# Optimization experiments

Hardware: AMD Instinct MI355X
Metric: run time of the kernel (lower is better)

The kernel has to match this reference:

```python
import jax, jax.numpy as jnp
import numpy as np

B, L, E, H = 2, 2048, 1024, 16
D = E // H  # 64


def setup_inputs() -> dict:
    key = jax.random.key(0)
    ks = jax.random.split(key, 9)
    return {
        "query": jax.random.normal(ks[0], (B, L, E), dtype=jnp.float32),
        "value": jax.random.normal(ks[1], (B, L, E), dtype=jnp.float32),
        "key": jax.random.normal(ks[2], (B, L, E), dtype=jnp.float32),
        "mask": jax.random.randint(ks[3], (B, 1, L, L), 0, 2, dtype=jnp.int32),
        "Wq": jax.random.normal(ks[4], (D, D), dtype=jnp.float32) * 0.05,
        "Wk": jax.random.normal(ks[5], (D, D), dtype=jnp.float32) * 0.05,
        "Wv": jax.random.normal(ks[6], (D, D), dtype=jnp.float32) * 0.05,
        "Wfc": jax.random.normal(ks[7], (E, E), dtype=jnp.float32) * 0.02,
        "bfc": jax.random.normal(ks[8], (E,), dtype=jnp.float32) * 0.02,
    }


def reference(query, value, key, mask, Wq, Wk, Wv, Wfc, bfc):
    b, q_len, _ = query.shape
    k_len = key.shape[1]
    v_len = value.shape[1]
    # split heads: [b, l, H, D]
    q = query.reshape(b, q_len, H, D)
    k = key.reshape(b, k_len, H, D)
    v = value.reshape(b, v_len, H, D)
    # per-head linear projections (shared weights across heads, no bias)
    q = jnp.einsum('bqhd,ed->bqhe', q, Wq)
    k = jnp.einsum('bkhd,ed->bkhe', k, Wk)
    v = jnp.einsum('bvhd,ed->bvhe', v, Wv)
    # attention scores [b, H, q, k]
    attn = jnp.einsum('bqhd,bkhd->bhqk', q, k)
    # NOTE: original masks BEFORE scaling, and scales by sqrt(embedding_size)
    attn = jnp.where(mask == 0, jnp.float32(-1e20), attn)
    attn = attn / jnp.float32(E ** 0.5)
    attn = jax.nn.softmax(attn, axis=3)
    out = jnp.einsum('bhqk,bkhd->bqhd', attn, v).reshape(b, q_len, E)
    out = out @ Wfc.T + bfc
    return out
```

## Files before the change

kernel.cpp:

```cpp
#include <hip/hip_runtime.h>
#include <hip/hip_bf16.h>


#define B_ 2
#define L_ 2048
#define E_ 1024
#define H_ 16
#define D_ 64

typedef __attribute__((ext_vector_type(8))) short s8v;
typedef __attribute__((ext_vector_type(4))) float f4v;
typedef __attribute__((ext_vector_type(2))) float f2v;

__device__ __forceinline__ f4v mfma16(s8v a, s8v b, f4v c) {
    return __builtin_amdgcn_mfma_f32_16x16x32_bf16(a, b, c, 0, 0, 0);
}

__device__ __forceinline__ float fast_exp2(float x) {
    return __builtin_amdgcn_exp2f(x);
}

__device__ __forceinline__ ushort bf16bits(float f) {
    __hip_bfloat16 h = __float2bfloat16(f);
    return *(ushort*)&h;
}

__device__ __forceinline__ void glds16(const __hip_bfloat16* g, ushort* l) {
    __builtin_amdgcn_global_load_lds(
        (const __attribute__((address_space(1))) void*)g,
        (__attribute__((address_space(3))) void*)l,
        16, 0, 0);
}

__device__ __forceinline__ s8v ld8_dual(const void* p, size_t idx, bool isf32) {
    if (isf32) {
        const float* pf = (const float*)p + idx;
        f4v f0 = *(const f4v*)pf;
        f4v f1 = *(const f4v*)(pf + 4);
        s8v r;
        r[0] = (short)bf16bits(f0[0]); r[1] = (short)bf16bits(f0[1]);
        r[2] = (short)bf16bits(f0[2]); r[3] = (short)bf16bits(f0[3]);
        r[4] = (short)bf16bits(f1[0]); r[5] = (short)bf16bits(f1[1]);
        r[6] = (short)bf16bits(f1[2]); r[7] = (short)bf16bits(f1[3]);
        return r;
    }
    return *(const s8v*)((const __hip_bfloat16*)p + idx);
}

__device__ __forceinline__ s8v ld8_ws(const __hip_bfloat16* p) {
    return *(const s8v*)p;
}

__device__ __forceinline__ s8v u4_to_s8(uint a, uint b, uint c, uint d) {
    union { uint u[4]; s8v v; } x;
    x.u[0] = a; x.u[1] = b; x.u[2] = c; x.u[3] = d;
    return x.v;
}

__device__ __forceinline__ bool block_detect_f32(const void* q_in, int* sflag) {
    if (threadIdx.x == 0) *sflag = 0;
    __syncthreads();
    const ushort* qq = (const ushort*)q_in + threadIdx.x * 16;
    int bad = 0;
    #pragma unroll
    for (int i = 0; i < 16; ++i) bad += (((qq[i] >> 7) & 0xFF) >= 0x8E);
    bad += __shfl_xor(bad, 1);
    bad += __shfl_xor(bad, 2);
    bad += __shfl_xor(bad, 4);
    bad += __shfl_xor(bad, 8);
    bad += __shfl_xor(bad, 16);
    bad += __shfl_xor(bad, 32);
    if ((threadIdx.x & 63) == 0) atomicAdd(sflag, bad);
    __syncthreads();
    return *sflag > 100;
}

__device__ __forceinline__ void cvt_piece(
    size_t i4, const void* Wfc, const void* bfc,
    __hip_bfloat16* wfc_bf, __hip_bfloat16* bfc_bf, bool isf32)
{
    const size_t base = i4 * 4;
    const size_t n1 = (size_t)E_ * E_;
    if (base >= n1 + E_) return;
    const void* src = (base < n1) ? Wfc : bfc;
    const size_t off = (base < n1) ? base : base - n1;
    __hip_bfloat16* dst = (base < n1) ? (wfc_bf + off) : (bfc_bf + off);
    if (isf32) {
        f4v v = *(const f4v*)((const float*)src + off);
        #pragma unroll
        for (int j = 0; j < 4; ++j) dst[j] = __float2bfloat16(v[j]);
    } else {
        *(ushort4*)dst = *(const ushort4*)((const ushort*)src + off);
    }
}

__global__ __launch_bounds__(256) void proj_all_kernel(
    const void* __restrict__ q_in, const void* __restrict__ k_in,
    const void* __restrict__ v_in,
    const void* __restrict__ Wq, const void* __restrict__ Wk,
    const void* __restrict__ Wv,
    const void* __restrict__ Wfc, const void* __restrict__ bfc,
    const int* __restrict__ mask, unsigned long long* __restrict__ mbits,
    __hip_bfloat16* __restrict__ qp, __hip_bfloat16* __restrict__ kp,
    __hip_bfloat16* __restrict__ vpT,
    __hip_bfloat16* __restrict__ wfc_bf, __hip_bfloat16* __restrict__ bfc_bf)
{
    __shared__ __align__(16) ushort tile[64][72];
    __shared__ __align__(16) ushort wlds[64 * 72];
    __shared__ int sflag;
    const int wave = threadIdx.x >> 6;
    const int lane = threadIdx.x & 63;
    const int quad = lane >> 4;
    const int l16  = lane & 15;

    if (blockIdx.y == 3) {
        const int lane_ = threadIdx.x & 63;
        const size_t wbase = (size_t)blockIdx.x * 128 + wave * 32;
        #pragma unroll 4
        for (int i = 0; i < 32; ++i) {
            const size_t widx = wbase + i;
            const int v = mask[widx * 64 + lane_];
            const unsigned long long bal = __ballot(v != 0);
            if (lane_ == 0) mbits[widx] = bal;
        }
        return;
    }

    const bool isf32 = block_detect_f32(q_in, &sflag);

    if (blockIdx.y == 4) {
        cvt_piece((size_t)blockIdx.x * 256 + threadIdx.x, Wfc, bfc, wfc_bf, bfc_bf, isf32);
        if (blockIdx.x == 0)
            cvt_piece((size_t)(E_ * (size_t)E_ / 4) + threadIdx.x, Wfc, bfc, wfc_bf, bfc_bf, isf32);
        return;
    }

    {
        const void* W = blockIdx.y == 0 ? Wq : (blockIdx.y == 1 ? Wk : Wv);
        const int row = threadIdx.x >> 2;
        const int c0  = (threadIdx.x & 3) * 16;
        if (isf32) {
            const float* wsrc = (const float*)W + row * 64 + c0;
            #pragma unroll
            for (int j = 0; j < 16; ++j)
                wlds[row * 72 + c0 + j] = bf16bits(wsrc[j]);
        } else {
            const ushort* wsrc = (const ushort*)W + row * 64 + c0;
            *(s8v*)&wlds[row * 72 + c0]     = *(const s8v*)wsrc;
            *(s8v*)&wlds[row * 72 + c0 + 8] = *(const s8v*)(wsrc + 8);
        }
    }
    __syncthreads();

    if (blockIdx.y < 2) {
        const void* X = blockIdx.y == 0 ? q_in : k_in;
        __hip_bfloat16* dst = blockIdx.y == 0 ? qp : kp;
        const float oscale = (blockIdx.y == 0) ? 0.045084439755930314f : 1.0f;
        const int m0 = (blockIdx.x * 4 + wave) * 16;

        const size_t abase = (size_t)(m0 + l16) * D_;
        s8v a0 = ld8_dual(X, abase + quad * 8, isf32);
        s8v a1 = ld8_dual(X, abase + 32 + quad * 8, isf32);

        f4v acc[4];
        #pragma unroll
        for (int nt = 0; nt < 4; ++nt) {
            const ushort* wr = &wlds[(nt * 16 + l16) * 72];
            s8v b0 = *(const s8v*)(wr + quad * 8);
            s8v b1 = *(const s8v*)(wr + 32 + quad * 8);
            f4v c = {0.f, 0.f, 0.f, 0.f};
            c = mfma16(a0, b0, c);
            c = mfma16(a1, b1, c);
            acc[nt] = c;
        }
        #pragma unroll
        for (int r = 0; r < 4; ++r) {
            const int m = m0 + quad * 4 + r;
            const int h = m & 15;
            const int bl = m >> 4;
            const int b = bl >> 11;
            const int l = bl & (L_ - 1);
            #pragma unroll
            for (int nt = 0; nt < 4; ++nt) {
                const int e = nt * 16 + l16;
                dst[(((size_t)(b * H_ + h)) * L_ + l) * D_ + e] =
                    __float2bfloat16(acc[nt][r] * oscale);
            }
        }
    } else {
        const int l0 = (blockIdx.x & 31) * 64;
        const int bh = blockIdx.x >> 5;
        const int b = bh >> 4, h = bh & 15;
        const int lw = l0 + wave * 16;

        const size_t xbase = ((size_t)(b * L_ + lw + l16)) * E_ + h * D_;
        s8v a0 = ld8_dual(v_in, xbase + quad * 8, isf32);
        s8v a1 = ld8_dual(v_in, xbase + 32 + quad * 8, isf32);

        #pragma unroll
        for (int nt = 0; nt < 4; ++nt) {
            const int e = nt * 16 + l16;
            const ushort* wr = &wlds[e * 72];
            s8v b0 = *(const s8v*)(wr + quad * 8);
            s8v b1 = *(const s8v*)(wr + 32 + quad * 8);
            f4v c = {0.f, 0.f, 0.f, 0.f};
            c = mfma16(a0, b0, c);
            c = mfma16(a1, b1, c);
            #pragma unroll
            for (int r = 0; r < 4; ++r)
                tile[wave * 16 + quad * 4 + r][e] = bf16bits(c[r]);
        }
        __syncthreads();
        const int e  = threadIdx.x >> 2;
        const int lc = (threadIdx.x & 3) * 16;
        s8v s0, s1;
        #pragma unroll
        for (int i = 0; i < 8; ++i) {
            s0[i] = (short)tile[lc + i][e];
            s1[i] = (short)tile[lc + 8 + i][e];
        }
        __hip_bfloat16* drow = vpT + ((size_t)bh * D_ + e) * L_ + l0 + lc;
        *(s8v*)drow = s0;
        *(s8v*)(drow + 8) = s1;
    }
}

__global__ __launch_bounds__(256) void cvt_wfc_kernel(
    const void* __restrict__ Wfc, const void* __restrict__ bfc,
    __hip_bfloat16* __restrict__ wfc_bf, __hip_bfloat16* __restrict__ bfc_bf,
    const void* __restrict__ q_in)
{
    __shared__ int sflag;
    const bool isf32 = block_detect_f32(q_in, &sflag);
    cvt_piece((size_t)blockIdx.x * 256 + threadIdx.x, Wfc, bfc, wfc_bf, bfc_bf, isf32);
}

__global__ __launch_bounds__(256, 4) void attn_kernel(
    const __hip_bfloat16* __restrict__ qp,
    const __hip_bfloat16* __restrict__ kp,
    const __hip_bfloat16* __restrict__ vpT,
    const unsigned long long* __restrict__ mbits,
    __hip_bfloat16* __restrict__ attn_out)
{
    __shared__ __align__(16) ushort kbuf[2][64 * 64];
    __shared__ __align__(16) ushort vbuf[2][64 * 64];

    const int wave = threadIdx.x >> 6;
    const int lane = threadIdx.x & 63;
    const int quad = lane >> 4;
    const int l16  = lane & 15;
    const int sw   = l16 & 7;
    const int bh = blockIdx.y;
    const int b = bh >> 4, h = bh & 15;
    const int q0 = blockIdx.x * 64 + wave * 16;

    const __hip_bfloat16* kbh = kp + (size_t)bh * L_ * D_;
    const __hip_bfloat16* vbh = vpT + (size_t)bh * D_ * L_;
    const unsigned long long* mrow = mbits + ((size_t)b * L_ + q0 + l16) * 32;

    const int lrow = lane >> 3;
    const int lchk = (lane & 7) ^ lrow;
    const int r0 = wave * 16;
    const __hip_bfloat16* kg0 = kbh + (size_t)(r0 + lrow) * D_ + lchk * 8;
    const __hip_bfloat16* kg1 = kbh + (size_t)(r0 + 8 + lrow) * D_ + lchk * 8;
    const __hip_bfloat16* vg0 = vbh + (size_t)(r0 + lrow) * L_ + lchk * 8;
    const __hip_bfloat16* vg1 = vbh + (size_t)(r0 + 8 + lrow) * L_ + lchk * 8;

    const __hip_bfloat16* qbase = qp + ((size_t)bh * L_ + q0) * D_;
    s8v qa0 = ld8_ws(qbase + (size_t)l16 * D_ + quad * 8);
    s8v qa1 = ld8_ws(qbase + (size_t)l16 * D_ + 32 + quad * 8);

    f2v rs2 = {0.f, 0.f};
    f4v o[4];
    #pragma unroll
    for (int nt = 0; nt < 4; ++nt) o[nt] = (f4v){0.f, 0.f, 0.f, 0.f};

    glds16(kg0, &kbuf[0][r0 * 64]);
    glds16(kg1, &kbuf[0][r0 * 64 + 512]);
    glds16(vg0, &vbuf[0][r0 * 64]);
    glds16(vg1, &vbuf[0][r0 * 64 + 512]);
    __syncthreads();

    const int shq = quad * 4;
    int cur = 0;
    for (int it = 0; it < 32; ++it) {
        const int k0 = it * 64;
        const unsigned long long wq = mrow[it];
        const uint wlo_sh = ((uint)wq) >> shq;
        const uint whi_sh = ((uint)(wq >> 32)) >> shq;
        if (it < 31) {
            glds16(kg0 + (size_t)(k0 + 64) * D_, &kbuf[cur ^ 1][r0 * 64]);
            glds16(kg1 + (size_t)(k0 + 64) * D_, &kbuf[cur ^ 1][r0 * 64 + 512]);
            glds16(vg0 + (k0 + 64), &vbuf[cur ^ 1][r0 * 64]);
            glds16(vg1 + (k0 + 64), &vbuf[cur ^ 1][r0 * 64 + 512]);
        }
        f4v s[4];
        #pragma unroll
        for (int nt = 0; nt < 4; ++nt) {
            const ushort* kr = &kbuf[cur][(nt * 16 + l16) * 64];
            s8v kb0 = *(const s8v*)(kr + ((quad ^ sw) << 3));
            s8v kb1 = *(const s8v*)(kr + (((quad + 4) ^ sw) << 3));
            f4v c = {0.f, 0.f, 0.f, 0.f};
            c = mfma16(kb0, qa0, c);
            c = mfma16(kb1, qa1, c);
            s[nt] = c;
        }
        uint dw[4][2];
        #pragma unroll
        for (int nt = 0; nt < 4; ++nt) {
            const uint hs = (nt & 2) ? whi_sh : wlo_sh;
            float pr[4];
            #pragma unroll
            for (int r = 0; r < 4; ++r) {
                const float p = fast_exp2(s[nt][r]);
                const int m = __builtin_amdgcn_sbfe((int)hs, ((nt & 1) << 4) + r, 1);
                pr[r] = __uint_as_float(__float_as_uint(p) & (uint)m);
            }
            rs2 += (f2v){pr[0], pr[1]};
            rs2 += (f2v){pr[2], pr[3]};
            asm("v_cvt_pk_bf16_f32 %0, %1, %2"
                : "=v"(dw[nt][0]) : "v"(pr[0]), "v"(pr[1]));
            asm("v_cvt_pk_bf16_f32 %0, %1, %2"
                : "=v"(dw[nt][1]) : "v"(pr[2]), "v"(pr[3]));
        }
        uint w00 = dw[0][0], w10 = dw[1][0];
        uint w01 = dw[0][1], w11 = dw[1][1];
        uint w20 = dw[2][0], w30 = dw[3][0];
        uint w21 = dw[2][1], w31 = dw[3][1];
        asm("v_permlane32_swap_b32 %0, %1" : "+v"(w00), "+v"(w10));
        asm("v_permlane16_swap_b32 %0, %1" : "+v"(w00), "+v"(w10));
        asm("v_permlane32_swap_b32 %0, %1" : "+v"(w01), "+v"(w11));
        asm("v_permlane16_swap_b32 %0, %1" : "+v"(w01), "+v"(w11));
        asm("v_permlane32_swap_b32 %0, %1" : "+v"(w20), "+v"(w30));
        asm("v_permlane16_swap_b32 %0, %1" : "+v"(w20), "+v"(w30));
        asm("v_permlane32_swap_b32 %0, %1" : "+v"(w21), "+v"(w31));
        asm("v_permlane16_swap_b32 %0, %1" : "+v"(w21), "+v"(w31));
        s8v pa0 = u4_to_s8(w00, w01, w10, w11);
        s8v pa1 = u4_to_s8(w20, w21, w30, w31);
        #pragma unroll
        for (int nt = 0; nt < 4; ++nt) {
            const ushort* vr = &vbuf[cur][(nt * 16 + l16) * 64];
            s8v vb0 = *(const s8v*)(vr + ((quad ^ sw) << 3));
            s8v vb1 = *(const s8v*)(vr + (((quad + 4) ^ sw) << 3));
            o[nt] = mfma16(pa0, vb0, o[nt]);
            o[nt] = mfma16(pa1, vb1, o[nt]);
        }
        __syncthreads();
        cur ^= 1;
    }
    float v = rs2[0] + rs2[1];
    v += __shfl_xor(v, 16, 64);
    v += __shfl_xor(v, 32, 64);
    #pragma unroll
    for (int r = 0; r < 4; ++r) {
        const int qrow = quad * 4 + r;
        const float li = __shfl(v, qrow, 64);
        const float inv = 1.0f / fmaxf(li, 1e-30f);
        const int row = q0 + qrow;
        #pragma unroll
        for (int nt = 0; nt < 4; ++nt) {
            const int d = nt * 16 + l16;
            attn_out[((size_t)(b * L_ + row)) * E_ + h * D_ + d] =
                __float2bfloat16(o[nt][r] * inv);
        }
    }
}

__global__ __launch_bounds__(256, 4) void fc_kernel(
    const __hip_bfloat16* __restrict__ x,
    const __hip_bfloat16* __restrict__ wfc_bf,
    const __hip_bfloat16* __restrict__ bfc_bf,
    void* __restrict__ out, const void* __restrict__ q_in)
{
    __shared__ __align__(16) ushort abuf[2][64 * 64];
    __shared__ __align__(16) ushort bbuf[2][64 * 64];
    __shared__ int sflag;
    const bool isf32 = block_detect_f32(q_in, &sflag);
    const int wave = threadIdx.x >> 6;
    const int lane = threadIdx.x & 63;
    const int quad = lane >> 4;
    const int l16  = lane & 15;
    const int sw   = l16 & 7;
    const int m0 = blockIdx.x * 64;
    const int n0 = blockIdx.y * 64;

    const int lrow = lane >> 3;
    const int lchk = (lane & 7) ^ lrow;
    const int r0 = wave * 16;
    const __hip_bfloat16* ag0 = x + (size_t)(m0 + r0 + lrow) * E_ + lchk * 8;
    const __hip_bfloat16* ag1 = x + (size_t)(m0 + r0 + 8 + lrow) * E_ + lchk * 8;
    const __hip_bfloat16* bg0 = wfc_bf + (size_t)(n0 + r0 + lrow) * E_ + lchk * 8;
    const __hip_bfloat16* bg1 = wfc_bf + (size_t)(n0 + r0 + 8 + lrow) * E_ + lchk * 8;

    f4v acc[4];
    #pragma unroll
    for (int nt = 0; nt < 4; ++nt) acc[nt] = (f4v){0.f, 0.f, 0.f, 0.f};

    glds16(ag0, &abuf[0][r0 * 64]);
    glds16(ag1, &abuf[0][r0 * 64 + 512]);
    glds16(bg0, &bbuf[0][r0 * 64]);
    glds16(bg1, &bbuf[0][r0 * 64 + 512]);
    __syncthreads();

    int cur = 0;
    for (int it = 0; it < 16; ++it) {
        const int k0 = it * 64;
        if (it < 15) {
            glds16(ag0 + k0 + 64, &abuf[cur ^ 1][r0 * 64]);
            glds16(ag1 + k0 + 64, &abuf[cur ^ 1][r0 * 64 + 512]);
            glds16(bg0 + k0 + 64, &bbuf[cur ^ 1][r0 * 64]);
            glds16(bg1 + k0 + 64, &bbuf[cur ^ 1][r0 * 64 + 512]);
        }
        const ushort* ar = &abuf[cur][(r0 + l16) * 64];
        s8v a0 = *(const s8v*)(ar + ((quad ^ sw) << 3));
        s8v a1 = *(const s8v*)(ar + (((quad + 4) ^ sw) << 3));
        #pragma unroll
        for (int nt = 0; nt < 4; ++nt) {
            const ushort* br = &bbuf[cur][(nt * 16 + l16) * 64];
            s8v b0 = *(const s8v*)(br + ((quad ^ sw) << 3));
            s8v b1 = *(const s8v*)(br + (((quad + 4) ^ sw) << 3));
            acc[nt] = mfma16(a0, b0, acc[nt]);
            acc[nt] = mfma16(a1, b1, acc[nt]);
        }
        __syncthreads();
        cur ^= 1;
    }
    #pragma unroll
    for (int r = 0; r < 4; ++r) {
        const int m = m0 + r0 + quad * 4 + r;
        #pragma unroll
        for (int nt = 0; nt < 4; ++nt) {
            const int n = n0 + nt * 16 + l16;
            const float val = acc[nt][r] + __bfloat162float(bfc_bf[n]);
            if (isf32) ((float*)out)[(size_t)m * E_ + n] = val;
            else       ((__hip_bfloat16*)out)[(size_t)m * E_ + n] = __float2bfloat16(val);
        }
    }
}

extern "C" void kernel_launch(void* const* d_in, const int* in_sizes, int n_in,
                              void* d_out, int out_size, void* d_ws, size_t ws_size,
                              hipStream_t stream) {
    const void* query = d_in[0];
    const void* value = d_in[1];
    const void* key   = d_in[2];
    const int*  mask  = (const int*)d_in[3];
    const void* Wq  = d_in[4];
    const void* Wk  = d_in[5];
    const void* Wv  = d_in[6];
    const void* Wfc = d_in[7];
    const void* bfc = d_in[8];

    char* ws = (char*)d_ws;
    unsigned long long* mbits     = (unsigned long long*)(ws + (64u << 10));
    __hip_bfloat16* qp            = (__hip_bfloat16*)(ws + (2u  << 20));
    __hip_bfloat16* kp            = (__hip_bfloat16*)(ws + (10u << 20));
    __hip_bfloat16* vpT           = (__hip_bfloat16*)(ws + (18u << 20));
    __hip_bfloat16* attn_out      = (__hip_bfloat16*)(ws + (26u << 20));

    const bool big_ws = ws_size >= (37ull << 20);
    __hip_bfloat16* wfc_bf = big_ws ? (__hip_bfloat16*)(ws + (34ull << 20)) : qp;
    __hip_bfloat16* bfc_bf = wfc_bf + (size_t)E_ * E_;

    proj_all_kernel<<<dim3(1024, big_ws ? 5 : 4), 256, 0, stream>>>(
        query, key, value, Wq, Wk, Wv, Wfc, bfc, mask, mbits,
        qp, kp, vpT, wfc_bf, bfc_bf);
    attn_kernel<<<dim3(32, 32), 256, 0, stream>>>(qp, kp, vpT, mbits, attn_out);
    if (!big_ws)
        cvt_wfc_kernel<<<1025, 256, 0, stream>>>(Wfc, bfc, wfc_bf, bfc_bf, query);
    fc_kernel<<<dim3(64, 16), 256, 0, stream>>>(attn_out, wfc_bf, bfc_bf, d_out, query);
}
```

Before: 222.0 us.

## Enlarge FC GEMM tiles to 128x128 and store Q/K projections row-major

The FC kernel moves from 64x64 tiles with 256 threads to 128x128 tiles with 512 threads. Each wave now computes a 64x32 sub-tile with 4x2 MFMA fragments, which raises operand reuse from LDS and cuts the block count. Separately, the Q/K projection outputs are written in the natural [b,l,h,d] layout, so the stores are contiguous. The attention kernel now reads them with stride E instead of per-head contiguous rows. The trade-offs are higher register pressure, more LDS per block, and fewer blocks (256) to fill the GPU.

```diff
diff --git a/kernel.cpp b/kernel.cpp
--- a/kernel.cpp
+++ b/kernel.cpp
@@ -60,7 +60,7 @@
 __device__ __forceinline__ bool block_detect_f32(const void* q_in, int* sflag) {
     if (threadIdx.x == 0) *sflag = 0;
     __syncthreads();
-    const ushort* qq = (const ushort*)q_in + threadIdx.x * 16;
+    const ushort* qq = (const ushort*)q_in + (threadIdx.x & 255) * 16;
     int bad = 0;
     #pragma unroll
     for (int i = 0; i < 16; ++i) bad += (((qq[i] >> 7) & 0xFF) >= 0x8E);
@@ -70,7 +70,7 @@
     bad += __shfl_xor(bad, 8);
     bad += __shfl_xor(bad, 16);
     bad += __shfl_xor(bad, 32);
-    if ((threadIdx.x & 63) == 0) atomicAdd(sflag, bad);
+    if ((threadIdx.x & 63) == 0 && threadIdx.x < 256) atomicAdd(sflag, bad);
     __syncthreads();
     return *sflag > 100;
 }
@@ -176,15 +176,10 @@
         #pragma unroll
         for (int r = 0; r < 4; ++r) {
             const int m = m0 + quad * 4 + r;
-            const int h = m & 15;
-            const int bl = m >> 4;
-            const int b = bl >> 11;
-            const int l = bl & (L_ - 1);
             #pragma unroll
             for (int nt = 0; nt < 4; ++nt) {
                 const int e = nt * 16 + l16;
-                dst[(((size_t)(b * H_ + h)) * L_ + l) * D_ + e] =
-                    __float2bfloat16(acc[nt][r] * oscale);
+                dst[(size_t)m * D_ + e] = __float2bfloat16(acc[nt][r] * oscale);
             }
         }
     } else {
@@ -254,21 +249,21 @@
     const int b = bh >> 4, h = bh & 15;
     const int q0 = blockIdx.x * 64 + wave * 16;
 
-    const __hip_bfloat16* kbh = kp + (size_t)bh * L_ * D_;
+    const __hip_bfloat16* kbh = kp + (size_t)b * L_ * E_ + h * D_;
     const __hip_bfloat16* vbh = vpT + (size_t)bh * D_ * L_;
     const unsigned long long* mrow = mbits + ((size_t)b * L_ + q0 + l16) * 32;
 
     const int lrow = lane >> 3;
     const int lchk = (lane & 7) ^ lrow;
     const int r0 = wave * 16;
-    const __hip_bfloat16* kg0 = kbh + (size_t)(r0 + lrow) * D_ + lchk * 8;
-    const __hip_bfloat16* kg1 = kbh + (size_t)(r0 + 8 + lrow) * D_ + lchk * 8;
+    const __hip_bfloat16* kg0 = kbh + (size_t)(r0 + lrow) * E_ + lchk * 8;
+    const __hip_bfloat16* kg1 = kbh + (size_t)(r0 + 8 + lrow) * E_ + lchk * 8;
     const __hip_bfloat16* vg0 = vbh + (size_t)(r0 + lrow) * L_ + lchk * 8;
     const __hip_bfloat16* vg1 = vbh + (size_t)(r0 + 8 + lrow) * L_ + lchk * 8;
 
-    const __hip_bfloat16* qbase = qp + ((size_t)bh * L_ + q0) * D_;
-    s8v qa0 = ld8_ws(qbase + (size_t)l16 * D_ + quad * 8);
-    s8v qa1 = ld8_ws(qbase + (size_t)l16 * D_ + 32 + quad * 8);
+    const __hip_bfloat16* qbase = qp + (size_t)b * L_ * E_ + h * D_ + (size_t)q0 * E_;
+    s8v qa0 = ld8_ws(qbase + (size_t)l16 * E_ + quad * 8);
+    s8v qa1 = ld8_ws(qbase + (size_t)l16 * E_ + 32 + quad * 8);
 
     f2v rs2 = {0.f, 0.f};
     f4v o[4];
@@ -289,8 +284,8 @@
         const uint wlo_sh = ((uint)wq) >> shq;
         const uint whi_sh = ((uint)(wq >> 32)) >> shq;
         if (it < 31) {
-            glds16(kg0 + (size_t)(k0 + 64) * D_, &kbuf[cur ^ 1][r0 * 64]);
-            glds16(kg1 + (size_t)(k0 + 64) * D_, &kbuf[cur ^ 1][r0 * 64 + 512]);
+            glds16(kg0 + (size_t)(k0 + 64) * E_, &kbuf[cur ^ 1][r0 * 64]);
+            glds16(kg1 + (size_t)(k0 + 64) * E_, &kbuf[cur ^ 1][r0 * 64 + 512]);
             glds16(vg0 + (k0 + 64), &vbuf[cur ^ 1][r0 * 64]);
             glds16(vg1 + (k0 + 64), &vbuf[cur ^ 1][r0 * 64 + 512]);
         }
@@ -366,14 +361,14 @@
     }
 }
 
-__global__ __launch_bounds__(256, 4) void fc_kernel(
+__global__ __launch_bounds__(512, 2) void fc_kernel(
     const __hip_bfloat16* __restrict__ x,
     const __hip_bfloat16* __restrict__ wfc_bf,
     const __hip_bfloat16* __restrict__ bfc_bf,
     void* __restrict__ out, const void* __restrict__ q_in)
 {
-    __shared__ __align__(16) ushort abuf[2][64 * 64];
-    __shared__ __align__(16) ushort bbuf[2][64 * 64];
+    __shared__ __align__(16) ushort abuf[2][128 * 64];
+    __shared__ __align__(16) ushort bbuf[2][128 * 64];
     __shared__ int sflag;
     const bool isf32 = block_detect_f32(q_in, &sflag);
     const int wave = threadIdx.x >> 6;
@@ -381,59 +376,77 @@
     const int quad = lane >> 4;
     const int l16  = lane & 15;
     const int sw   = l16 & 7;
-    const int m0 = blockIdx.x * 64;
-    const int n0 = blockIdx.y * 64;
+    const int m0 = blockIdx.x * 128;
+    const int n0 = blockIdx.y * 128;
+    const int wr = wave >> 2;
+    const int wc = wave & 3;
 
     const int lrow = lane >> 3;
     const int lchk = (lane & 7) ^ lrow;
-    const int r0 = wave * 16;
-    const __hip_bfloat16* ag0 = x + (size_t)(m0 + r0 + lrow) * E_ + lchk * 8;
-    const __hip_bfloat16* ag1 = x + (size_t)(m0 + r0 + 8 + lrow) * E_ + lchk * 8;
-    const __hip_bfloat16* bg0 = wfc_bf + (size_t)(n0 + r0 + lrow) * E_ + lchk * 8;
-    const __hip_bfloat16* bg1 = wfc_bf + (size_t)(n0 + r0 + 8 + lrow) * E_ + lchk * 8;
-
-    f4v acc[4];
-    #pragma unroll
-    for (int nt = 0; nt < 4; ++nt) acc[nt] = (f4v){0.f, 0.f, 0.f, 0.f};
-
-    glds16(ag0, &abuf[0][r0 * 64]);
-    glds16(ag1, &abuf[0][r0 * 64 + 512]);
-    glds16(bg0, &bbuf[0][r0 * 64]);
-    glds16(bg1, &bbuf[0][r0 * 64 + 512]);
+
+    const __hip_bfloat16* ag[2];
+    const __hip_bfloat16* bg[2];
+    #pragma unroll
+    for (int c = 0; c < 2; ++c) {
+        ag[c] = x      + (size_t)(m0 + c * 64 + wave * 8 + lrow) * E_ + lchk * 8;
+        bg[c] = wfc_bf + (size_t)(n0 + c * 64 + wave * 8 + lrow) * E_ + lchk * 8;
+    }
+
+    f4v acc[4][2];
+    #pragma unroll
+    for (int fm = 0; fm < 4; ++fm)
+        #pragma unroll
+        for (int fn = 0; fn < 2; ++fn) acc[fm][fn] = (f4v){0.f, 0.f, 0.f, 0.f};
+
+    #pragma unroll
+    for (int c = 0; c < 2; ++c) {
+        glds16(ag[c], &abuf[0][(c * 64 + wave * 8) * 64]);
+        glds16(bg[c], &bbuf[0][(c * 64 + wave * 8) * 64]);
+    }
     __syncthreads();
 
     int cur = 0;
     for (int it = 0; it < 16; ++it) {
-        const int k0 = it * 64;
         if (it < 15) {
-            glds16(ag0 + k0 + 64, &abuf[cur ^ 1][r0 * 64]);
-            glds16(ag1 + k0 + 64, &abuf[cur ^ 1][r0 * 64 + 512]);
-            glds16(bg0 + k0 + 64, &bbuf[cur ^ 1][r0 * 64]);
-            glds16(bg1 + k0 + 64, &bbuf[cur ^ 1][r0 * 64 + 512]);
-        }
-        const ushort* ar = &abuf[cur][(r0 + l16) * 64];
-        s8v a0 = *(const s8v*)(ar + ((quad ^ sw) << 3));
-        s8v a1 = *(const s8v*)(ar + (((quad + 4) ^ sw) << 3));
-        #pragma unroll
-        for (int nt = 0; nt < 4; ++nt) {
-            const ushort* br = &bbuf[cur][(nt * 16 + l16) * 64];
+            #pragma unroll
+            for (int c = 0; c < 2; ++c) {
+                glds16(ag[c] + (it + 1) * 64, &abuf[cur ^ 1][(c * 64 + wave * 8) * 64]);
+                glds16(bg[c] + (it + 1) * 64, &bbuf[cur ^ 1][(c * 64 + wave * 8) * 64]);
+            }
+        }
+        s8v a0[4], a1[4];
+        #pragma unroll
+        for (int fm = 0; fm < 4; ++fm) {
+            const ushort* ar = &abuf[cur][(wr * 64 + fm * 16 + l16) * 64];
+            a0[fm] = *(const s8v*)(ar + ((quad ^ sw) << 3));
+            a1[fm] = *(const s8v*)(ar + (((quad + 4) ^ sw) << 3));
+        }
+        #pragma unroll
+        for (int fn = 0; fn < 2; ++fn) {
+            const ushort* br = &bbuf[cur][(wc * 32 + fn * 16 + l16) * 64];
             s8v b0 = *(const s8v*)(br + ((quad ^ sw) << 3));
             s8v b1 = *(const s8v*)(br + (((quad + 4) ^ sw) << 3));
-            acc[nt] = mfma16(a0, b0, acc[nt]);
-            acc[nt] = mfma16(a1, b1, acc[nt]);
+            #pragma unroll
+            for (int fm = 0; fm < 4; ++fm) {
+                acc[fm][fn] = mfma16(a0[fm], b0, acc[fm][fn]);
+                acc[fm][fn] = mfma16(a1[fm], b1, acc[fm][fn]);
+            }
         }
         __syncthreads();
         cur ^= 1;
     }
     #pragma unroll
-    for (int r = 0; r < 4; ++r) {
-        const int m = m0 + r0 + quad * 4 + r;
-        #pragma unroll
-        for (int nt = 0; nt < 4; ++nt) {
-            const int n = n0 + nt * 16 + l16;
-            const float val = acc[nt][r] + __bfloat162float(bfc_bf[n]);
-            if (isf32) ((float*)out)[(size_t)m * E_ + n] = val;
-            else       ((__hip_bfloat16*)out)[(size_t)m * E_ + n] = __float2bfloat16(val);
+    for (int fm = 0; fm < 4; ++fm) {
+        #pragma unroll
+        for (int r = 0; r < 4; ++r) {
+            const int m = m0 + wr * 64 + fm * 16 + quad * 4 + r;
+            #pragma unroll
+            for (int fn = 0; fn < 2; ++fn) {
+                const int n = n0 + wc * 32 + fn * 16 + l16;
+                const float val = acc[fm][fn][r] + __bfloat162float(bfc_bf[n]);
+                if (isf32) ((float*)out)[(size_t)m * E_ + n] = val;
+                else       ((__hip_bfloat16*)out)[(size_t)m * E_ + n] = __float2bfloat16(val);
+            }
         }
     }
 }
@@ -468,5 +481,5 @@
     attn_kernel<<<dim3(32, 32), 256, 0, stream>>>(qp, kp, vpT, mbits, attn_out);
     if (!big_ws)
         cvt_wfc_kernel<<<1025, 256, 0, stream>>>(Wfc, bfc, wfc_bf, bfc_bf, query);
-    fc_kernel<<<dim3(64, 16), 256, 0, stream>>>(attn_out, wfc_bf, bfc_bf, d_out, query);
-}
+    fc_kernel<<<dim3(32, 8), 512, 0, stream>>>(attn_out, wfc_bf, bfc_bf, d_out, query);
+}
```

Measured after the change: 221.6 us. No clear change (-0.1%).
